# Performance work log

Hardware: AMD Instinct MI355X
Metric: run time of the kernel (lower is better)

## Reference

```python
import jax, jax.numpy as jnp
import numpy as np

B, S, E, H = 2, 2048, 1024, 16
D = E // H

def setup_inputs() -> dict:
    key = jax.random.key(0)
    ks = jax.random.split(key, 5)
    return {
        "hidden_states": jax.random.normal(ks[0], (B, S, E), dtype=jnp.float32),
        "c_attn_w": jax.random.normal(ks[1], (E, 3 * E), dtype=jnp.float32) * 0.02,
        "c_attn_b": jax.random.normal(ks[2], (3 * E,), dtype=jnp.float32) * 0.02,
        "c_proj_w": jax.random.normal(ks[3], (E, E), dtype=jnp.float32) * 0.02,
        "c_proj_b": jax.random.normal(ks[4], (E,), dtype=jnp.float32) * 0.02,
    }

def reference(hidden_states, c_attn_w, c_attn_b, c_proj_w, c_proj_b):
    x = hidden_states                      # [B, S, E]
    b, s, _ = x.shape
    w_q, w_k, w_v = jnp.split(c_attn_w, 3, axis=1)   # each [E, E]
    q_b, k_b, v_b = jnp.split(c_attn_b, 3, axis=0)   # each [E]

    # value projection
    v = x @ w_v + v_b                                        # [B,S,E]
    v = v.reshape(b, s, H, D).transpose(0, 2, 1, 3)          # [B,H,S,D]

    # fused query: ((x Wq + qb) Wk^T + kb)
    q = (x @ w_q + q_b) @ w_k.T + k_b                        # [B,S,E]
    qh = q.reshape(b, s, H, D).transpose(0, 2, 1, 3)         # [B,H,S,D]

    # key side is RAW hidden states split per head
    kh = x.reshape(b, s, H, D).transpose(0, 2, 1, 3)         # [B,H,S,D]

    scale = 1.0 / jnp.float32(D) ** 0.5
    scores = jnp.einsum("bhqd,bhkd->bhqk",
                        qh.astype(jnp.float32),
                        kh.astype(jnp.float32)) * scale       # [B,H,S,S] fp32

    causal = jnp.tril(jnp.ones((s, s), dtype=bool))
    mask_value = jnp.finfo(jnp.float32).min
    scores = jnp.where(causal[None, None], scores, mask_value)

    probs = jax.nn.softmax(scores, axis=-1).astype(v.dtype)  # [B,H,S,S]

    out = jnp.einsum("bhqk,bhkd->bhqd", probs, v)            # [B,H,S,D]
    out = out.transpose(0, 2, 1, 3).reshape(b, s, E)         # [B,S,E]
    out = out @ c_proj_w + c_proj_b
    return out
```

## Files before the change

kernel.cpp:

```cpp
#include <hip/hip_runtime.h>

typedef __attribute__((ext_vector_type(8))) __bf16 bf16x8;
typedef __attribute__((ext_vector_type(4))) __bf16 bf16x4;
typedef __attribute__((ext_vector_type(4))) float f32x4;

typedef __attribute__((address_space(1))) void as1_void;
typedef __attribute__((address_space(3))) void as3_void;

__device__ __forceinline__ void gl_lds16(const void* g, void* l) {
    __builtin_amdgcn_global_load_lds((const as1_void*)g, (as3_void*)l, 16, 0, 0);
}

__device__ __forceinline__ const bf16x8* swz(const __bf16* base, int row, int chunk) {
    return (const bf16x8*)((const char*)base + row * 128 + ((chunk ^ (row & 7)) * 16));
}

#define QSCALE (0.125f * 1.44269504f)

__global__ __launch_bounds__(256) void prep_kernel(
    const float* __restrict__ x, const float* __restrict__ caw,
    const float* __restrict__ cpw,
    __bf16* __restrict__ xb, __bf16* __restrict__ wvt,
    __bf16* __restrict__ wpt, __bf16* __restrict__ wqt,
    __bf16* __restrict__ wkn)
{
    __shared__ float tile[32 * 33];
    int bid = blockIdx.x;
    int tid = threadIdx.x;
    if (bid < 1024) {
        int nt = bid >> 5, kt = bid & 31;
        int tx = tid & 31, ty = tid >> 5;
        int n0 = nt * 32, k0 = kt * 32;
#pragma unroll
        for (int i = 0; i < 4; ++i)
            tile[(ty + i * 8) * 33 + tx] = caw[(long)(k0 + ty + i * 8) * 3072 + 2048 + n0 + tx];
        __syncthreads();
#pragma unroll
        for (int i = 0; i < 4; ++i)
            wvt[(long)(n0 + ty + i * 8) * 1024 + k0 + tx] = (__bf16)tile[tx * 33 + ty + i * 8];
    } else if (bid < 2048) {
        int v = bid - 1024;
        int nt = v >> 5, kt = v & 31;
        int tx = tid & 31, ty = tid >> 5;
        int n0 = nt * 32, k0 = kt * 32;
#pragma unroll
        for (int i = 0; i < 4; ++i)
            tile[(ty + i * 8) * 33 + tx] = cpw[(long)(k0 + ty + i * 8) * 1024 + n0 + tx];
        __syncthreads();
#pragma unroll
        for (int i = 0; i < 4; ++i)
            wpt[(long)(n0 + ty + i * 8) * 1024 + k0 + tx] = (__bf16)tile[tx * 33 + ty + i * 8];
    } else if (bid < 3072) {
        int v = bid - 2048;
        int nt = v >> 5, kt = v & 31;
        int tx = tid & 31, ty = tid >> 5;
        int n0 = nt * 32, k0 = kt * 32;
#pragma unroll
        for (int i = 0; i < 4; ++i)
            tile[(ty + i * 8) * 33 + tx] = caw[(long)(k0 + ty + i * 8) * 3072 + n0 + tx];
        __syncthreads();
#pragma unroll
        for (int i = 0; i < 4; ++i)
            wqt[(long)(n0 + ty + i * 8) * 1024 + k0 + tx] = (__bf16)tile[tx * 33 + ty + i * 8];
    } else if (bid < 4096) {
        int e = (bid - 3072) * 1024 + tid * 4;
        int n = e >> 10, k = e & 1023;
        float4 f = *(const float4*)(caw + (long)n * 3072 + 1024 + k);
        bf16x4 o = {(__bf16)f.x, (__bf16)f.y, (__bf16)f.z, (__bf16)f.w};
        *(bf16x4*)(wkn + e) = o;
    } else {
        long e = (long)(bid - 4096) * 1024 + tid * 4;
        float4 f = *(const float4*)(x + e);
        bf16x4 o = {(__bf16)f.x, (__bf16)f.y, (__bf16)f.z, (__bf16)f.w};
        *(bf16x4*)(xb + e) = o;
    }
}

__global__ __launch_bounds__(256) void gemm_tv(
    const __bf16* __restrict__ xb, const __bf16* __restrict__ wqt,
    const __bf16* __restrict__ wvt, const float* __restrict__ cab,
    __bf16* __restrict__ tb, __bf16* __restrict__ vt)
{
    __shared__ __bf16 smem[128 * 136];
    const int bid = blockIdx.x;
    const int tid = threadIdx.x;
    const int lane = tid & 63;
    const int wave = tid >> 6;
    const int quad = lane >> 4, l16 = lane & 15;

    if (bid < 512) {
        __bf16* As = smem;
        __bf16* Bs = smem + 8192;
        const int bx = bid & 15, by = bid >> 4;
        const long m0 = (long)by * 128;
        const long n0 = (long)bx * 64;
        const int wm = (wave >> 1) * 64, wn = (wave & 1) * 32;

        f32x4 acc[4][2] = {};
        for (int k0 = 0; k0 < 1024; k0 += 64) {
#pragma unroll
            for (int c = tid; c < 1536; c += 256) {
                int row = c >> 3, cc = (c & 7) ^ (row & 7);
                if (row < 128)
                    gl_lds16(xb + (m0 + row) * 1024 + k0 + cc * 8, As + c * 8);
                else
                    gl_lds16(wqt + (n0 + row - 128) * 1024 + k0 + cc * 8, Bs + (c - 1024) * 8);
            }
            __syncthreads();
#pragma unroll
            for (int kk = 0; kk < 2; ++kk) {
                bf16x8 af[4], bfr[2];
#pragma unroll
                for (int i = 0; i < 4; ++i)
                    af[i] = *swz(As, wm + i * 16 + l16, kk * 4 + quad);
#pragma unroll
                for (int j = 0; j < 2; ++j)
                    bfr[j] = *swz(Bs, wn + j * 16 + l16, kk * 4 + quad);
#pragma unroll
                for (int i = 0; i < 4; ++i)
#pragma unroll
                    for (int j = 0; j < 2; ++j)
                        acc[i][j] = __builtin_amdgcn_mfma_f32_16x16x32_bf16(af[i], bfr[j], acc[i][j], 0, 0, 0);
            }
            __syncthreads();
        }
#pragma unroll
        for (int i = 0; i < 4; ++i) {
            long row = m0 + wm + i * 16 + quad * 4;
#pragma unroll
            for (int j = 0; j < 2; ++j) {
                int col = (int)n0 + wn + j * 16 + l16;
                float bb = cab[col];
#pragma unroll
                for (int r = 0; r < 4; ++r)
                    tb[(row + r) * 1024 + col] = (__bf16)(acc[i][j][r] + bb);
            }
        }
    } else {
        __bf16* As = smem;
        __bf16* Bs = smem + 8192;
        const int v2 = bid - 512;
        const int bx = v2 & 7, by = v2 >> 3;
        const long m0 = (long)by * 128;
        const long n0 = (long)bx * 128;
        const int wm = (wave >> 1) * 64, wn = (wave & 1) * 64;

        f32x4 acc[4][4] = {};
        for (int k0 = 0; k0 < 1024; k0 += 64) {
#pragma unroll
            for (int c = tid; c < 2048; c += 256) {
                int row = c >> 3, cc = (c & 7) ^ (row & 7);
                if (row < 128)
                    gl_lds16(xb + (m0 + row) * 1024 + k0 + cc * 8, As + c * 8);
                else
                    gl_lds16(wvt + (n0 + row - 128) * 1024 + k0 + cc * 8, Bs + (c - 1024) * 8);
            }
            __syncthreads();
#pragma unroll
            for (int kk = 0; kk < 2; ++kk) {
                bf16x8 af[4], bfr[4];
#pragma unroll
                for (int i = 0; i < 4; ++i)
                    af[i] = *swz(As, wm + i * 16 + l16, kk * 4 + quad);
#pragma unroll
                for (int j = 0; j < 4; ++j)
                    bfr[j] = *swz(Bs, wn + j * 16 + l16, kk * 4 + quad);
#pragma unroll
                for (int i = 0; i < 4; ++i)
#pragma unroll
                    for (int j = 0; j < 4; ++j)
                        acc[i][j] = __builtin_amdgcn_mfma_f32_16x16x32_bf16(af[i], bfr[j], acc[i][j], 0, 0, 0);
            }
            __syncthreads();
        }
        __syncthreads();
#pragma unroll
        for (int i = 0; i < 4; ++i) {
#pragma unroll
            for (int j = 0; j < 4; ++j) {
                int col = (int)n0 + wn + j * 16 + l16;
                float bb = cab[2048 + col];
                bf16x4 v;
#pragma unroll
                for (int r = 0; r < 4; ++r) v[r] = (__bf16)(acc[i][j][r] + bb);
                *(bf16x4*)(smem + (wn + j * 16 + l16) * 136 + wm + i * 16 + quad * 4) = v;
            }
        }
        __syncthreads();
        const int bb2 = (int)(m0 >> 11);
        const int sl = (int)(m0 & 2047);
#pragma unroll
        for (int pass = 0; pass < 16; ++pass) {
            int idx = pass * 256 + tid;
            int n = idx >> 5;
            int mc = (idx & 31) * 4;
            bf16x4 v = *(const bf16x4*)(smem + n * 136 + mc);
            *(bf16x4*)(vt + ((long)(bb2 * 1024 + (int)n0 + n)) * 2048 + sl + mc) = v;
        }
    }
}

__global__ __launch_bounds__(512) void attn_kernel(
    const __bf16* __restrict__ T,
    const __bf16* __restrict__ Xb,
    const __bf16* __restrict__ VT,
    const __bf16* __restrict__ WK,
    const float* __restrict__ cab,
    __bf16* __restrict__ O)
{
    __shared__ __bf16 SM[40960];
    __bf16* Ks = SM;
    __bf16* Vs = SM + 16384;
    __bf16* Ps = SM + 32768;
    const int tid = threadIdx.x;
    const int lane = tid & 63;
    const int wave = tid >> 6;
    const int group = wave >> 2;
    const int w4 = wave & 3;
    const int quad = lane >> 4, l16 = lane & 15;
    const int qa = blockIdx.y;
    const int qb = 31 - qa;
    const int qt = group ? qb : qa;
    const int bh = blockIdx.x;
    const int b = bh >> 4, h = bh & 15;
    const long rowbase = (long)b * 2048;

    const int s0 = tid;
    const int c0 = ((s0 & 7) ^ ((s0 >> 3) & 7)) * 8;

    bf16x8 ones;
#pragma unroll
    for (int i = 0; i < 8; ++i) ones[i] = (__bf16)1.0f;

    bf16x8 qfr[2];
    {
        auto stage_q = [&](int ki, int buf) {
            __bf16* Ad = SM + buf * 8192;
            __bf16* Bd = SM + 24576 + buf * 4096;
#pragma unroll
            for (int u = 0; u < 3; ++u) {
                int c = tid + u * 512;
                if (c < 1024) {
                    int lr = c >> 3;
                    int cc = (c & 7) ^ (lr & 7);
                    int grow = (lr < 64) ? qa * 64 + lr : qb * 64 + (lr - 64);
                    gl_lds16(T + (rowbase + grow) * 1024 + ki * 64 + cc * 8, Ad + c * 8);
                } else {
                    int w = c - 1024;
                    int lr = w >> 3;
                    int cc = (w & 7) ^ (lr & 7);
                    gl_lds16(WK + (long)(h * 64 + lr) * 1024 + ki * 64 + cc * 8, Bd + w * 8);
                }
            }
        };

        f32x4 qacc[4] = {};
        stage_q(0, 0);
        for (int ki = 0; ki < 16; ++ki) {
            if (ki < 15) {
                stage_q(ki + 1, (ki + 1) % 3);
                asm volatile("s_waitcnt vmcnt(3)" ::: "memory");
            } else {
                asm volatile("s_waitcnt vmcnt(0)" ::: "memory");
            }
            __builtin_amdgcn_sched_barrier(0);
            __builtin_amdgcn_s_barrier();
            const __bf16* Aq = SM + (ki % 3) * 8192;
            const __bf16* Bq = SM + 24576 + (ki % 3) * 4096;
#pragma unroll
            for (int kk = 0; kk < 2; ++kk) {
                bf16x8 af = *swz(Aq + group * 4096, w4 * 16 + l16, kk * 4 + quad);
#pragma unroll
                for (int dt = 0; dt < 4; ++dt) {
                    bf16x8 bfr = *swz(Bq, dt * 16 + l16, kk * 4 + quad);
                    qacc[dt] = __builtin_amdgcn_mfma_f32_16x16x32_bf16(af, bfr, qacc[dt], 0, 0, 0);
                }
            }
        }
#pragma unroll
        for (int dt = 0; dt < 4; ++dt) {
            int d = dt * 16 + l16;
            float bb = cab[1024 + h * 64 + d];
#pragma unroll
            for (int r = 0; r < 4; ++r) {
                int row = group * 64 + w4 * 16 + quad * 4 + r;
                float v = (qacc[dt][r] + bb) * QSCALE;
                *(__bf16*)((char*)Ps + row * 128 + (((d >> 3) ^ (row & 7)) * 16) + (d & 7) * 2) = (__bf16)v;
            }
        }
        __syncthreads();
        qfr[0] = *swz(Ps + group * 4096, w4 * 16 + l16, quad);
        qfr[1] = *swz(Ps + group * 4096, w4 * 16 + l16, 4 + quad);
    }

    const __bf16* kp0 = Xb + (rowbase + (s0 >> 3)) * 1024 + h * 64 + c0;
    const __bf16* vp0 = VT + ((long)(b * 1024 + h * 64 + (s0 >> 3))) * 2048 + c0;

    auto stage_tile = [&](int j, int buf, int sub) {
        gl_lds16(kp0 + (long)j * 65536, Ks + buf * 8192 + sub * 4096 + s0 * 8);
        gl_lds16(vp0 + j * 64, Vs + buf * 8192 + sub * 4096 + s0 * 8);
    };
    stage_tile(0, 0, 0);
    stage_tile(1, 0, 1);

    const int nouter = (qb + 2) >> 1;

    f32x4 oacc[4] = {};
    f32x4 lacc = {};
    __bf16* Pw = Ps + wave * 1024;

    for (int jj = 0; jj < nouter; ++jj) {
        __syncthreads();
        if (jj + 1 < nouter) {
            stage_tile(2 * jj + 2, (jj + 1) & 1, 0);
            stage_tile(2 * jj + 3, (jj + 1) & 1, 1);
        }

#pragma unroll
        for (int sub = 0; sub < 2; ++sub) {
            const int j = 2 * jj + sub;
            if (j > qt) continue;
            const __bf16* Kb = Ks + (jj & 1) * 8192 + sub * 4096;
            const __bf16* Vb = Vs + (jj & 1) * 8192 + sub * 4096;

            bf16x8 kf[2][4], vf[2][4];
#pragma unroll
            for (int kk = 0; kk < 2; ++kk)
#pragma unroll
                for (int kt = 0; kt < 4; ++kt) {
                    kf[kk][kt] = *swz(Kb, kt * 16 + l16, kk * 4 + quad);
                    vf[kk][kt] = *swz(Vb, kt * 16 + l16, kk * 4 + quad);
                }

            f32x4 sacc[4] = {};
            __builtin_amdgcn_s_setprio(1);
#pragma unroll
            for (int kk = 0; kk < 2; ++kk)
#pragma unroll
                for (int kt = 0; kt < 4; ++kt)
                    sacc[kt] = __builtin_amdgcn_mfma_f32_16x16x32_bf16(
                        kf[kk][kt], qfr[kk], sacc[kt], 0, 0, 0);
            __builtin_amdgcn_s_setprio(0);

            if (j == qt) {
                const int qloc = w4 * 16 + l16;
#pragma unroll
                for (int kt = 0; kt < 4; ++kt) {
                    bf16x4 pk;
#pragma unroll
                    for (int r = 0; r < 4; ++r) {
                        float s = sacc[kt][r];
                        if (kt * 16 + quad * 4 + r > qloc) s = -1e30f;
                        pk[r] = (__bf16)exp2f(s);
                    }
                    *(bf16x4*)((char*)Pw + l16 * 128 +
                               (((kt * 2 + (quad >> 1)) ^ (l16 & 7)) * 16) + (quad & 1) * 8) = pk;
                }
            } else {
#pragma unroll
                for (int kt = 0; kt < 4; ++kt) {
                    bf16x4 pk;
#pragma unroll
                    for (int r = 0; r < 4; ++r)
                        pk[r] = (__bf16)exp2f(sacc[kt][r]);
                    *(bf16x4*)((char*)Pw + l16 * 128 +
                               (((kt * 2 + (quad >> 1)) ^ (l16 & 7)) * 16) + (quad & 1) * 8) = pk;
                }
            }

            __builtin_amdgcn_s_setprio(1);
#pragma unroll
            for (int kk = 0; kk < 2; ++kk) {
                bf16x8 pf = *swz(Pw, l16, kk * 4 + quad);
                lacc = __builtin_amdgcn_mfma_f32_16x16x32_bf16(ones, pf, lacc, 0, 0, 0);
#pragma unroll
                for (int dt = 0; dt < 4; ++dt)
                    oacc[dt] = __builtin_amdgcn_mfma_f32_16x16x32_bf16(
                        vf[kk][dt], pf, oacc[dt], 0, 0, 0);
            }
            __builtin_amdgcn_s_setprio(0);
        }
    }

    {
        float inv = 1.0f / lacc[0];
        long row = rowbase + qt * 64 + w4 * 16 + l16;
#pragma unroll
        for (int dt = 0; dt < 4; ++dt) {
            bf16x4 ov;
#pragma unroll
            for (int r = 0; r < 4; ++r) ov[r] = (__bf16)(oacc[dt][r] * inv);
            *(bf16x4*)(O + row * 1024 + h * 64 + dt * 16 + quad * 4) = ov;
        }
    }
}

__global__ __launch_bounds__(256) void gemm_proj(
    const __bf16* __restrict__ A, const __bf16* __restrict__ B,
    const float* __restrict__ bias, float* __restrict__ C)
{
    __shared__ __bf16 As[128 * 64];
    __shared__ __bf16 Bs[64 * 64];
    const int tid = threadIdx.x;
    const int lane = tid & 63;
    const int wave = tid >> 6;
    const int quad = lane >> 4, l16 = lane & 15;
    const long m0 = (long)blockIdx.y * 128;
    const long n0 = (long)blockIdx.x * 64;
    const int wm = (wave >> 1) * 64, wn = (wave & 1) * 32;

    f32x4 acc[4][2] = {};

    for (int k0 = 0; k0 < 1024; k0 += 64) {
#pragma unroll
        for (int c = tid; c < 1536; c += 256) {
            int row = c >> 3, cc = (c & 7) ^ (row & 7);
            if (row < 128)
                gl_lds16(A + (m0 + row) * 1024 + k0 + cc * 8, As + c * 8);
            else
                gl_lds16(B + (n0 + row - 128) * 1024 + k0 + cc * 8, Bs + (c - 1024) * 8);
        }
        __syncthreads();
#pragma unroll
        for (int kk = 0; kk < 2; ++kk) {
            bf16x8 af[4], bfr[2];
#pragma unroll
            for (int i = 0; i < 4; ++i)
                af[i] = *swz(As, wm + i * 16 + l16, kk * 4 + quad);
#pragma unroll
            for (int j = 0; j < 2; ++j)
                bfr[j] = *swz(Bs, wn + j * 16 + l16, kk * 4 + quad);
#pragma unroll
            for (int i = 0; i < 4; ++i)
#pragma unroll
                for (int j = 0; j < 2; ++j)
                    acc[i][j] = __builtin_amdgcn_mfma_f32_16x16x32_bf16(af[i], bfr[j], acc[i][j], 0, 0, 0);
        }
        __syncthreads();
    }
#pragma unroll
    for (int i = 0; i < 4; ++i) {
        long row = m0 + wm + i * 16 + quad * 4;
#pragma unroll
        for (int j = 0; j < 2; ++j) {
            int col = (int)n0 + wn + j * 16 + l16;
            float bb = bias[col];
#pragma unroll
            for (int r = 0; r < 4; ++r)
                C[(row + r) * 1024 + col] = acc[i][j][r] + bb;
        }
    }
}

extern "C" void kernel_launch(void* const* d_in, const int* in_sizes, int n_in,
                              void* d_out, int out_size, void* d_ws, size_t ws_size,
                              hipStream_t stream) {
    const float* x   = (const float*)d_in[0];
    const float* caw = (const float*)d_in[1];
    const float* cab = (const float*)d_in[2];
    const float* cpw = (const float*)d_in[3];
    const float* cpb = (const float*)d_in[4];

    char* p = (char*)d_ws;
    auto alloc = [&](size_t bytes) {
        void* r = (void*)p;
        p += (bytes + 255) & ~(size_t)255;
        return r;
    };
    __bf16* xb    = (__bf16*)alloc(4096UL * 1024 * 2);
    __bf16* wkn   = (__bf16*)alloc(1024UL * 1024 * 2);
    __bf16* wvt   = (__bf16*)alloc(1024UL * 1024 * 2);
    __bf16* wqt   = (__bf16*)alloc(1024UL * 1024 * 2);
    __bf16* wpt   = (__bf16*)alloc(1024UL * 1024 * 2);
    __bf16* tb    = (__bf16*)alloc(4096UL * 1024 * 2);
    __bf16* abuf  = (__bf16*)alloc(4096UL * 1024 * 2);
    __bf16* vt    = (__bf16*)alloc(2048UL * 2048 * 2);

    prep_kernel<<<8192, 256, 0, stream>>>(x, caw, cpw, xb, wvt, wpt, wqt, wkn);
    gemm_tv<<<768, 256, 0, stream>>>(xb, wqt, wvt, cab, tb, vt);
    attn_kernel<<<dim3(32, 16), 512, 0, stream>>>(tb, xb, vt, wkn, cab, abuf);
    gemm_proj<<<dim3(16, 32), 256, 0, stream>>>(abuf, wpt, cpb, (float*)d_out);
    (void)in_sizes; (void)n_in; (void)out_size; (void)ws_size;
}
```

Measured before the change: 181.1 us.

## Fuse weight conversion into Q and V projection GEMM kernel

Merges the prep and projection GEMM kernels into one launch. The Q/V GEMM blocks now read fp32 x and fp32 c_attn weights directly, converting and transposing them in LDS, so the separate wqt/wvt transposed bf16 copies and one kernel launch are dropped. The V GEMM also moves from 128x128 to 128x64 tiles so Q and V blocks share one code path. The cost is extra per-iteration conversion work, an added barrier, and twice the fp32 global traffic for the x tiles, which are re-read by every column block.

```diff
diff --git a/kernel.cpp b/kernel.cpp
--- a/kernel.cpp
+++ b/kernel.cpp
@@ -15,30 +15,125 @@
     return (const bf16x8*)((const char*)base + row * 128 + ((chunk ^ (row & 7)) * 16));
 }
 
+__device__ __forceinline__ bf16x8 cvt8(const float* p) {
+    float4 a = *(const float4*)p, b = *(const float4*)(p + 4);
+    bf16x8 o;
+    o[0] = (__bf16)a.x; o[1] = (__bf16)a.y; o[2] = (__bf16)a.z; o[3] = (__bf16)a.w;
+    o[4] = (__bf16)b.x; o[5] = (__bf16)b.y; o[6] = (__bf16)b.z; o[7] = (__bf16)b.w;
+    return o;
+}
+
 #define QSCALE (0.125f * 1.44269504f)
 
-__global__ __launch_bounds__(256) void prep_kernel(
+__global__ __launch_bounds__(256) void prep_tv(
     const float* __restrict__ x, const float* __restrict__ caw,
-    const float* __restrict__ cpw,
-    __bf16* __restrict__ xb, __bf16* __restrict__ wvt,
-    __bf16* __restrict__ wpt, __bf16* __restrict__ wqt,
-    __bf16* __restrict__ wkn)
+    const float* __restrict__ cpw, const float* __restrict__ cab,
+    __bf16* __restrict__ xb, __bf16* __restrict__ wkn,
+    __bf16* __restrict__ wpt, __bf16* __restrict__ tb,
+    __bf16* __restrict__ vt)
 {
-    __shared__ float tile[32 * 33];
-    int bid = blockIdx.x;
-    int tid = threadIdx.x;
+    __shared__ __bf16 SM[20480];
+    const int bid = blockIdx.x;
+    const int tid = threadIdx.x;
+
     if (bid < 1024) {
-        int nt = bid >> 5, kt = bid & 31;
-        int tx = tid & 31, ty = tid >> 5;
-        int n0 = nt * 32, k0 = kt * 32;
-#pragma unroll
-        for (int i = 0; i < 4; ++i)
-            tile[(ty + i * 8) * 33 + tx] = caw[(long)(k0 + ty + i * 8) * 3072 + 2048 + n0 + tx];
-        __syncthreads();
-#pragma unroll
-        for (int i = 0; i < 4; ++i)
-            wvt[(long)(n0 + ty + i * 8) * 1024 + k0 + tx] = (__bf16)tile[tx * 33 + ty + i * 8];
+        __bf16* As = SM;
+        __bf16* Bs = SM + 8192;
+        float*  ft = (float*)(SM + 12288);
+        const bool isv = bid >= 512;
+        const int v2 = isv ? bid - 512 : bid;
+        const int bx = v2 & 15, by = v2 >> 4;
+        const long m0 = (long)by * 128;
+        const int n0 = bx * 64;
+        const int nbase = isv ? 2048 + n0 : n0;
+        const int lane = tid & 63, wave = tid >> 6;
+        const int quad = lane >> 4, l16 = lane & 15;
+        const int wm = (wave >> 1) * 64, wn = (wave & 1) * 32;
+
+        f32x4 acc[4][2] = {};
+
+        for (int k0 = 0; k0 < 1024; k0 += 64) {
+            __syncthreads();
+#pragma unroll
+            for (int u = tid; u < 1024; u += 256)
+                gl_lds16(caw + (long)(k0 + (u >> 4)) * 3072 + nbase + (u & 15) * 4,
+                         SM + 12288 + u * 8);
+#pragma unroll
+            for (int u = tid; u < 1024; u += 256) {
+                int row = u >> 3, p = u & 7;
+                int sc = p ^ (row & 7);
+                bf16x8 o = cvt8(x + (m0 + row) * 1024 + k0 + sc * 8);
+                *(bf16x8*)(As + u * 8) = o;
+            }
+            __syncthreads();
+#pragma unroll
+            for (int w = tid; w < 512; w += 256) {
+                int n = w & 63, chunk = w >> 6;
+                bf16x8 o;
+#pragma unroll
+                for (int i = 0; i < 8; ++i)
+                    o[i] = (__bf16)ft[(chunk * 8 + i) * 64 + n];
+                *(bf16x8*)((char*)Bs + n * 128 + ((chunk ^ (n & 7)) * 16)) = o;
+            }
+            __syncthreads();
+#pragma unroll
+            for (int kk = 0; kk < 2; ++kk) {
+                bf16x8 af[4], bfr[2];
+#pragma unroll
+                for (int i = 0; i < 4; ++i)
+                    af[i] = *swz(As, wm + i * 16 + l16, kk * 4 + quad);
+#pragma unroll
+                for (int j = 0; j < 2; ++j)
+                    bfr[j] = *swz(Bs, wn + j * 16 + l16, kk * 4 + quad);
+#pragma unroll
+                for (int i = 0; i < 4; ++i)
+#pragma unroll
+                    for (int j = 0; j < 2; ++j)
+                        acc[i][j] = __builtin_amdgcn_mfma_f32_16x16x32_bf16(af[i], bfr[j], acc[i][j], 0, 0, 0);
+            }
+        }
+
+        if (!isv) {
+#pragma unroll
+            for (int i = 0; i < 4; ++i) {
+                long row = m0 + wm + i * 16 + quad * 4;
+#pragma unroll
+                for (int j = 0; j < 2; ++j) {
+                    int col = n0 + wn + j * 16 + l16;
+                    float bb = cab[col];
+#pragma unroll
+                    for (int r = 0; r < 4; ++r)
+                        tb[(row + r) * 1024 + col] = (__bf16)(acc[i][j][r] + bb);
+                }
+            }
+        } else {
+            __syncthreads();
+#pragma unroll
+            for (int i = 0; i < 4; ++i) {
+#pragma unroll
+                for (int j = 0; j < 2; ++j) {
+                    int cl = wn + j * 16 + l16;
+                    float bb = cab[2048 + n0 + cl];
+                    bf16x4 v;
+#pragma unroll
+                    for (int r = 0; r < 4; ++r) v[r] = (__bf16)(acc[i][j][r] + bb);
+                    *(bf16x4*)(SM + cl * 136 + wm + i * 16 + quad * 4) = v;
+                }
+            }
+            __syncthreads();
+            const int bb2 = (int)(m0 >> 11);
+            const int sl = (int)(m0 & 2047);
+#pragma unroll
+            for (int pass = 0; pass < 8; ++pass) {
+                int idx = pass * 256 + tid;
+                int n = idx >> 5;
+                int mc = (idx & 31) * 4;
+                bf16x4 v = *(const bf16x4*)(SM + n * 136 + mc);
+                *(bf16x4*)(vt + ((long)(bb2 * 1024 + n0 + n)) * 2048 + sl + mc) = v;
+            }
+        }
     } else if (bid < 2048) {
+        float* tile = (float*)SM;
         int v = bid - 1024;
         int nt = v >> 5, kt = v & 31;
         int tx = tid & 31, ty = tid >> 5;
@@ -51,152 +146,16 @@
         for (int i = 0; i < 4; ++i)
             wpt[(long)(n0 + ty + i * 8) * 1024 + k0 + tx] = (__bf16)tile[tx * 33 + ty + i * 8];
     } else if (bid < 3072) {
-        int v = bid - 2048;
-        int nt = v >> 5, kt = v & 31;
-        int tx = tid & 31, ty = tid >> 5;
-        int n0 = nt * 32, k0 = kt * 32;
-#pragma unroll
-        for (int i = 0; i < 4; ++i)
-            tile[(ty + i * 8) * 33 + tx] = caw[(long)(k0 + ty + i * 8) * 3072 + n0 + tx];
-        __syncthreads();
-#pragma unroll
-        for (int i = 0; i < 4; ++i)
-            wqt[(long)(n0 + ty + i * 8) * 1024 + k0 + tx] = (__bf16)tile[tx * 33 + ty + i * 8];
-    } else if (bid < 4096) {
-        int e = (bid - 3072) * 1024 + tid * 4;
+        int e = (bid - 2048) * 1024 + tid * 4;
         int n = e >> 10, k = e & 1023;
         float4 f = *(const float4*)(caw + (long)n * 3072 + 1024 + k);
         bf16x4 o = {(__bf16)f.x, (__bf16)f.y, (__bf16)f.z, (__bf16)f.w};
         *(bf16x4*)(wkn + e) = o;
     } else {
-        long e = (long)(bid - 4096) * 1024 + tid * 4;
+        long e = (long)(bid - 3072) * 1024 + tid * 4;
         float4 f = *(const float4*)(x + e);
         bf16x4 o = {(__bf16)f.x, (__bf16)f.y, (__bf16)f.z, (__bf16)f.w};
         *(bf16x4*)(xb + e) = o;
-    }
-}
-
-__global__ __launch_bounds__(256) void gemm_tv(
-    const __bf16* __restrict__ xb, const __bf16* __restrict__ wqt,
-    const __bf16* __restrict__ wvt, const float* __restrict__ cab,
-    __bf16* __restrict__ tb, __bf16* __restrict__ vt)
-{
-    __shared__ __bf16 smem[128 * 136];
-    const int bid = blockIdx.x;
-    const int tid = threadIdx.x;
-    const int lane = tid & 63;
-    const int wave = tid >> 6;
-    const int quad = lane >> 4, l16 = lane & 15;
-
-    if (bid < 512) {
-        __bf16* As = smem;
-        __bf16* Bs = smem + 8192;
-        const int bx = bid & 15, by = bid >> 4;
-        const long m0 = (long)by * 128;
-        const long n0 = (long)bx * 64;
-        const int wm = (wave >> 1) * 64, wn = (wave & 1) * 32;
-
-        f32x4 acc[4][2] = {};
-        for (int k0 = 0; k0 < 1024; k0 += 64) {
-#pragma unroll
-            for (int c = tid; c < 1536; c += 256) {
-                int row = c >> 3, cc = (c & 7) ^ (row & 7);
-                if (row < 128)
-                    gl_lds16(xb + (m0 + row) * 1024 + k0 + cc * 8, As + c * 8);
-                else
-                    gl_lds16(wqt + (n0 + row - 128) * 1024 + k0 + cc * 8, Bs + (c - 1024) * 8);
-            }
-            __syncthreads();
-#pragma unroll
-            for (int kk = 0; kk < 2; ++kk) {
-                bf16x8 af[4], bfr[2];
-#pragma unroll
-                for (int i = 0; i < 4; ++i)
-                    af[i] = *swz(As, wm + i * 16 + l16, kk * 4 + quad);
-#pragma unroll
-                for (int j = 0; j < 2; ++j)
-                    bfr[j] = *swz(Bs, wn + j * 16 + l16, kk * 4 + quad);
-#pragma unroll
-                for (int i = 0; i < 4; ++i)
-#pragma unroll
-                    for (int j = 0; j < 2; ++j)
-                        acc[i][j] = __builtin_amdgcn_mfma_f32_16x16x32_bf16(af[i], bfr[j], acc[i][j], 0, 0, 0);
-            }
-            __syncthreads();
-        }
-#pragma unroll
-        for (int i = 0; i < 4; ++i) {
-            long row = m0 + wm + i * 16 + quad * 4;
-#pragma unroll
-            for (int j = 0; j < 2; ++j) {
-                int col = (int)n0 + wn + j * 16 + l16;
-                float bb = cab[col];
-#pragma unroll
-                for (int r = 0; r < 4; ++r)
-                    tb[(row + r) * 1024 + col] = (__bf16)(acc[i][j][r] + bb);
-            }
-        }
-    } else {
-        __bf16* As = smem;
-        __bf16* Bs = smem + 8192;
-        const int v2 = bid - 512;
-        const int bx = v2 & 7, by = v2 >> 3;
-        const long m0 = (long)by * 128;
-        const long n0 = (long)bx * 128;
-        const int wm = (wave >> 1) * 64, wn = (wave & 1) * 64;
-
-        f32x4 acc[4][4] = {};
-        for (int k0 = 0; k0 < 1024; k0 += 64) {
-#pragma unroll
-            for (int c = tid; c < 2048; c += 256) {
-                int row = c >> 3, cc = (c & 7) ^ (row & 7);
-                if (row < 128)
-                    gl_lds16(xb + (m0 + row) * 1024 + k0 + cc * 8, As + c * 8);
-                else
-                    gl_lds16(wvt + (n0 + row - 128) * 1024 + k0 + cc * 8, Bs + (c - 1024) * 8);
-            }
-            __syncthreads();
-#pragma unroll
-            for (int kk = 0; kk < 2; ++kk) {
-                bf16x8 af[4], bfr[4];
-#pragma unroll
-                for (int i = 0; i < 4; ++i)
-                    af[i] = *swz(As, wm + i * 16 + l16, kk * 4 + quad);
-#pragma unroll
-                for (int j = 0; j < 4; ++j)
-                    bfr[j] = *swz(Bs, wn + j * 16 + l16, kk * 4 + quad);
-#pragma unroll
-                for (int i = 0; i < 4; ++i)
-#pragma unroll
-                    for (int j = 0; j < 4; ++j)
-                        acc[i][j] = __builtin_amdgcn_mfma_f32_16x16x32_bf16(af[i], bfr[j], acc[i][j], 0, 0, 0);
-            }
-            __syncthreads();
-        }
-        __syncthreads();
-#pragma unroll
-        for (int i = 0; i < 4; ++i) {
-#pragma unroll
-            for (int j = 0; j < 4; ++j) {
-                int col = (int)n0 + wn + j * 16 + l16;
-                float bb = cab[2048 + col];
-                bf16x4 v;
-#pragma unroll
-                for (int r = 0; r < 4; ++r) v[r] = (__bf16)(acc[i][j][r] + bb);
-                *(bf16x4*)(smem + (wn + j * 16 + l16) * 136 + wm + i * 16 + quad * 4) = v;
-            }
-        }
-        __syncthreads();
-        const int bb2 = (int)(m0 >> 11);
-        const int sl = (int)(m0 & 2047);
-#pragma unroll
-        for (int pass = 0; pass < 16; ++pass) {
-            int idx = pass * 256 + tid;
-            int n = idx >> 5;
-            int mc = (idx & 31) * 4;
-            bf16x4 v = *(const bf16x4*)(smem + n * 136 + mc);
-            *(bf16x4*)(vt + ((long)(bb2 * 1024 + (int)n0 + n)) * 2048 + sl + mc) = v;
-        }
     }
 }
 
@@ -469,15 +428,12 @@
     };
     __bf16* xb    = (__bf16*)alloc(4096UL * 1024 * 2);
     __bf16* wkn   = (__bf16*)alloc(1024UL * 1024 * 2);
-    __bf16* wvt   = (__bf16*)alloc(1024UL * 1024 * 2);
-    __bf16* wqt   = (__bf16*)alloc(1024UL * 1024 * 2);
     __bf16* wpt   = (__bf16*)alloc(1024UL * 1024 * 2);
     __bf16* tb    = (__bf16*)alloc(4096UL * 1024 * 2);
     __bf16* abuf  = (__bf16*)alloc(4096UL * 1024 * 2);
     __bf16* vt    = (__bf16*)alloc(2048UL * 2048 * 2);
 
-    prep_kernel<<<8192, 256, 0, stream>>>(x, caw, cpw, xb, wvt, wpt, wqt, wkn);
-    gemm_tv<<<768, 256, 0, stream>>>(xb, wqt, wvt, cab, tb, vt);
+    prep_tv<<<7168, 256, 0, stream>>>(x, caw, cpw, cab, xb, wkn, wpt, tb, vt);
     attn_kernel<<<dim3(32, 16), 512, 0, stream>>>(tb, xb, vt, wkn, cab, abuf);
     gemm_proj<<<dim3(16, 32), 256, 0, stream>>>(abuf, wpt, cpb, (float*)d_out);
     (void)in_sizes; (void)n_in; (void)out_size; (void)ws_size;
```

Measured after the change: 186.0 us. +2.7%, slower.
